# Kernel optimization log

Hardware: AMD Instinct MI355X
Metric: run time of the kernel (lower is better)

The kernel has to match this reference:

```python
import jax, jax.numpy as jnp
import numpy as np

N = 100000
E = 1600000
IN_CH = 165
H1 = 128
H2 = 64
OUT = 2


def gcn_conv(x, W, b, src, dst, n):
    # PyG GCNConv: linear transform, add self-loops, symmetric normalization,
    # scatter-add aggregation, then bias.
    h = x @ W  # [n, out_ch]
    ones = jnp.ones(src.shape[0], dtype=h.dtype)
    deg = jax.ops.segment_sum(ones, dst, num_segments=n) + 1.0  # +1 for self-loop
    dinv = jax.lax.rsqrt(deg)
    norm = dinv[src] * dinv[dst]  # [E]
    agg = jax.ops.segment_sum(h[src] * norm[:, None], dst, num_segments=n)
    agg = agg + (dinv * dinv)[:, None] * h  # self-loop contribution
    return agg + b


def setup_inputs() -> dict:
    key = jax.random.key(0)
    ks = jax.random.split(key, 8)
    x = jax.random.normal(ks[0], (N, IN_CH), dtype=jnp.float32)
    edge_index = jax.random.randint(ks[1], (2, E), 0, N, dtype=jnp.int32)
    W1 = jax.random.normal(ks[2], (IN_CH, H1), dtype=jnp.float32) * (1.0 / np.sqrt(IN_CH))
    b1 = jnp.zeros((H1,), dtype=jnp.float32)
    W2 = jax.random.normal(ks[3], (H1, H2), dtype=jnp.float32) * (1.0 / np.sqrt(H1))
    b2 = jnp.zeros((H2,), dtype=jnp.float32)
    Wo = jax.random.normal(ks[4], (H2, OUT), dtype=jnp.float32) * (1.0 / np.sqrt(H2))
    bo = jnp.zeros((OUT,), dtype=jnp.float32)
    return {"x": x, "edge_index": edge_index, "W1": W1, "b1": b1,
            "W2": W2, "b2": b2, "Wo": Wo, "bo": bo}


def reference(x, edge_index, W1, b1, W2, b2, Wo, bo):
    src, dst = edge_index[0], edge_index[1]
    n = x.shape[0]
    h = jax.nn.relu(gcn_conv(x, W1, b1, src, dst, n))
    h = jax.nn.relu(gcn_conv(h, W2, b2, src, dst, n))
    return h @ Wo + bo  # [N, 2] logits
```

## Files before the change

### kernel.cpp

```cpp
#include <hip/hip_runtime.h>
#include <hip/hip_fp16.h>

#define N_NODES 100000
#define N_EDGES 1600000
#define IN_CH 165
#define H1C 128
#define H2C 64
#define K1PAD 192
#define CAP 64
#define SCATTER_BLOCKS 2048
#define PART_SZ 12500
#define GEMM1_BLOCKS ((N_NODES + 63) / 64)

typedef _Float16 half8 __attribute__((ext_vector_type(8)));
typedef float floatx4 __attribute__((ext_vector_type(4)));

__global__ __launch_bounds__(256) void prep(const float* __restrict__ W1,
                                            const float* __restrict__ W2,
                                            int* __restrict__ cnt,
                                            _Float16* __restrict__ w1t,
                                            _Float16* __restrict__ w2t) {
    int i = blockIdx.x * 256 + threadIdx.x;
    if (i < N_NODES) cnt[i] = 0;
    if (i < H1C * K1PAD) {
        int c = i / K1PAD, k = i - c * K1PAD;
        w1t[i] = (k < IN_CH) ? (_Float16)W1[k * H1C + c] : (_Float16)0.0f;
    }
    if (i < H2C * H1C) {
        int c = i >> 7, k = i & 127;
        w2t[i] = (_Float16)W2[k * H2C + c];
    }
}

__global__ void dinv_from_cnt(const int* __restrict__ cnt, float* __restrict__ dinv) {
    int i = blockIdx.x * 256 + threadIdx.x;
    if (i < N_NODES) dinv[i] = rsqrtf((float)cnt[i] + 1.0f);
}

__global__ __launch_bounds__(256) void scatter_and_gemm1(
        const int* __restrict__ ei, int* __restrict__ cnt, int* __restrict__ csr,
        const float* __restrict__ x, const _Float16* __restrict__ w1t,
        _Float16* __restrict__ h1) {
    __shared__ _Float16 lsA[64 * 200];
    int tid = threadIdx.x;

    if (blockIdx.x < SCATTER_BLOCKS) {
        int g  = blockIdx.x & 7;
        int bg = blockIdx.x >> 3;
        int lo = g * PART_SZ;
        int hi = lo + PART_SZ;
        const int* dstp = ei + N_EDGES;
        for (int e = bg * 256 + tid; e < N_EDGES; e += (SCATTER_BLOCKS / 8) * 256) {
            int d = dstp[e];
            if (d >= lo && d < hi) {
                int s = ei[e];
                int pos = atomicAdd(&cnt[d], 1);
                if (pos < CAP) csr[(d << 6) + pos] = s;
            }
        }
        return;
    }

    int bid = blockIdx.x - SCATTER_BLOCKS;
    int row0 = bid * 64;

    const int TILE_EL = 64 * IN_CH;
    int base = row0 * IN_CH;
    for (int idx = tid; idx < TILE_EL; idx += 256) {
        int r = idx / IN_CH;
        int k = idx - r * IN_CH;
        int g = base + idx;
        float v = (g < N_NODES * IN_CH) ? x[g] : 0.0f;
        lsA[r * 200 + k] = (_Float16)v;
    }
    for (int idx = tid; idx < 64 * 35; idx += 256) {
        int r = idx / 35;
        int k = IN_CH + (idx - r * 35);
        lsA[r * 200 + k] = (_Float16)0.0f;
    }
    __syncthreads();

    int lane = tid & 63;
    int w = tid >> 6;
    int m = lane & 15;
    int q = lane >> 4;

    floatx4 acc[4][2] = {};
#pragma unroll
    for (int ks = 0; ks < 6; ++ks) {
        half8 af[4];
#pragma unroll
        for (int mt = 0; mt < 4; ++mt)
            af[mt] = *(const half8*)&lsA[(mt * 16 + m) * 200 + ks * 32 + q * 8];
        half8 bf[2];
#pragma unroll
        for (int nt = 0; nt < 2; ++nt)
            bf[nt] = *(const half8*)&w1t[((w * 2 + nt) * 16 + m) * K1PAD + ks * 32 + q * 8];
#pragma unroll
        for (int mt = 0; mt < 4; ++mt)
#pragma unroll
            for (int nt = 0; nt < 2; ++nt)
                acc[mt][nt] = __builtin_amdgcn_mfma_f32_16x16x32_f16(af[mt], bf[nt], acc[mt][nt], 0, 0, 0);
    }

#pragma unroll
    for (int mt = 0; mt < 4; ++mt) {
#pragma unroll
        for (int nt = 0; nt < 2; ++nt) {
            int col = (w * 2 + nt) * 16 + m;
#pragma unroll
            for (int reg = 0; reg < 4; ++reg) {
                int row = row0 + mt * 16 + q * 4 + reg;
                if (row < N_NODES) h1[(size_t)row * H1C + col] = (_Float16)acc[mt][nt][reg];
            }
        }
    }
}

__global__ __launch_bounds__(256) void gemm2_mfma(const _Float16* __restrict__ A,
                                                  const _Float16* __restrict__ w2t,
                                                  _Float16* __restrict__ h2) {
    __shared__ _Float16 lsA[64 * 136];
    int tid = threadIdx.x;
    int row0 = blockIdx.x * 64;

    const uint* srcu = (const uint*)(A + (size_t)row0 * H1C);
    for (int idx = tid; idx < 4096; idx += 256) {
        int r = idx >> 6;
        int kp = idx & 63;
        uint v = ((size_t)(row0 + r) < (size_t)N_NODES) ? srcu[idx] : 0u;
        *(uint*)&lsA[r * 136 + kp * 2] = v;
    }
    __syncthreads();

    int lane = tid & 63;
    int w = tid >> 6;
    int m = lane & 15;
    int q = lane >> 4;

    floatx4 acc[4] = {};
#pragma unroll
    for (int ks = 0; ks < 4; ++ks) {
        half8 bf = *(const half8*)&w2t[(w * 16 + m) * H1C + ks * 32 + q * 8];
#pragma unroll
        for (int mt = 0; mt < 4; ++mt) {
            half8 af = *(const half8*)&lsA[(mt * 16 + m) * 136 + ks * 32 + q * 8];
            acc[mt] = __builtin_amdgcn_mfma_f32_16x16x32_f16(af, bf, acc[mt], 0, 0, 0);
        }
    }

    int col = w * 16 + m;
#pragma unroll
    for (int mt = 0; mt < 4; ++mt) {
#pragma unroll
        for (int reg = 0; reg < 4; ++reg) {
            int row = row0 + mt * 16 + q * 4 + reg;
            if (row < N_NODES) h2[(size_t)row * H2C + col] = (_Float16)acc[mt][reg];
        }
    }
}

__global__ __launch_bounds__(256) void agg_gather_128(const __half* __restrict__ h,
                                                      const float* __restrict__ dinv,
                                                      const int* __restrict__ cnt,
                                                      const int* __restrict__ csr,
                                                      const float* __restrict__ b,
                                                      __half* __restrict__ out) {
    const __half2* hp = (const __half2*)h;
    int wave = threadIdx.x >> 6;
    int lane = threadIdx.x & 63;
    int node = blockIdx.x * 4 + wave;
    if (node >= N_NODES) return;
    int deg = min(cnt[node], CAP);
    const int* cp = csr + ((size_t)node << 6);
    float di = dinv[node];
    float ax = 0.0f, ay = 0.0f;
    int e = 0;
    for (; e + 3 < deg; e += 4) {
        int s0 = cp[e], s1 = cp[e + 1], s2 = cp[e + 2], s3 = cp[e + 3];
        float n0 = dinv[s0], n1 = dinv[s1], n2 = dinv[s2], n3 = dinv[s3];
        float2 v0 = __half22float2(hp[(size_t)s0 * 64 + lane]);
        float2 v1 = __half22float2(hp[(size_t)s1 * 64 + lane]);
        float2 v2 = __half22float2(hp[(size_t)s2 * 64 + lane]);
        float2 v3 = __half22float2(hp[(size_t)s3 * 64 + lane]);
        ax += v0.x * n0 + v1.x * n1 + v2.x * n2 + v3.x * n3;
        ay += v0.y * n0 + v1.y * n1 + v2.y * n2 + v3.y * n3;
    }
    for (; e < deg; ++e) {
        int s0 = cp[e];
        float n0 = dinv[s0];
        float2 v0 = __half22float2(hp[(size_t)s0 * 64 + lane]);
        ax += v0.x * n0;
        ay += v0.y * n0;
    }
    float2 hv = __half22float2(hp[(size_t)node * 64 + lane]);
    float2 bv = *(const float2*)&b[lane * 2];
    float ox = fmaxf(ax * di + di * di * hv.x + bv.x, 0.0f);
    float oy = fmaxf(ay * di + di * di * hv.y + bv.y, 0.0f);
    ((__half2*)out)[(size_t)node * 64 + lane] = __floats2half2_rn(ox, oy);
}

__global__ __launch_bounds__(256) void agg_gather_64_final(const __half* __restrict__ h,
                                                           const float* __restrict__ dinv,
                                                           const int* __restrict__ cnt,
                                                           const int* __restrict__ csr,
                                                           const float* __restrict__ b,
                                                           const float* __restrict__ Wo,
                                                           const float* __restrict__ bo,
                                                           float* __restrict__ out) {
    int wave = threadIdx.x >> 6;
    int lane = threadIdx.x & 63;
    int node = blockIdx.x * 4 + wave;
    if (node >= N_NODES) return;
    int deg = min(cnt[node], CAP);
    const int* cp = csr + ((size_t)node << 6);
    float di = dinv[node];
    float acc = 0.0f;
    int e = 0;
    for (; e + 3 < deg; e += 4) {
        int s0 = cp[e], s1 = cp[e + 1], s2 = cp[e + 2], s3 = cp[e + 3];
        float n0 = dinv[s0], n1 = dinv[s1], n2 = dinv[s2], n3 = dinv[s3];
        float v0 = __half2float(h[(size_t)s0 * H2C + lane]);
        float v1 = __half2float(h[(size_t)s1 * H2C + lane]);
        float v2 = __half2float(h[(size_t)s2 * H2C + lane]);
        float v3 = __half2float(h[(size_t)s3 * H2C + lane]);
        acc += v0 * n0 + v1 * n1 + v2 * n2 + v3 * n3;
    }
    for (; e < deg; ++e) {
        int s0 = cp[e];
        acc += __half2float(h[(size_t)s0 * H2C + lane]) * dinv[s0];
    }
    float hv = __half2float(h[(size_t)node * H2C + lane]);
    float v = fmaxf(acc * di + di * di * hv + b[lane], 0.0f);
    float a0 = v * Wo[lane * 2];
    float a1 = v * Wo[lane * 2 + 1];
#pragma unroll
    for (int off = 32; off > 0; off >>= 1) {
        a0 += __shfl_down(a0, off, 64);
        a1 += __shfl_down(a1, off, 64);
    }
    if (lane == 0) {
        *(float2*)&out[(size_t)node * 2] = make_float2(a0 + bo[0], a1 + bo[1]);
    }
}

static inline char* align256(char* p) {
    return (char*)(((uintptr_t)p + 255) & ~(uintptr_t)255);
}

extern "C" void kernel_launch(void* const* d_in, const int* in_sizes, int n_in,
                              void* d_out, int out_size, void* d_ws, size_t ws_size,
                              hipStream_t stream) {
    const float* x  = (const float*)d_in[0];
    const int*   ei = (const int*)d_in[1];
    const float* W1 = (const float*)d_in[2];
    const float* b1 = (const float*)d_in[3];
    const float* W2 = (const float*)d_in[4];
    const float* b2 = (const float*)d_in[5];
    const float* Wo = (const float*)d_in[6];
    const float* bo = (const float*)d_in[7];
    float* out = (float*)d_out;

    char* wp = (char*)d_ws;
    int* cnt      = (int*)wp;        wp = align256(wp + sizeof(int) * N_NODES);
    int* csr      = (int*)wp;        wp = align256(wp + sizeof(int) * (size_t)N_NODES * CAP);
    float* dinv   = (float*)wp;      wp = align256(wp + sizeof(float) * N_NODES);
    _Float16* w1t = (_Float16*)wp;   wp = align256(wp + sizeof(_Float16) * H1C * K1PAD);
    _Float16* w2t = (_Float16*)wp;   wp = align256(wp + sizeof(_Float16) * H2C * H1C);
    _Float16* h1h = (_Float16*)wp;   wp = align256(wp + sizeof(_Float16) * (size_t)N_NODES * H1C);
    _Float16* a1h = (_Float16*)wp;   wp = align256(wp + sizeof(_Float16) * (size_t)N_NODES * H1C);
    _Float16* h2h = (_Float16*)wp;   wp = align256(wp + sizeof(_Float16) * (size_t)N_NODES * H2C);

    const int nb_n   = (N_NODES + 255) / 256;
    const int nb_nd4 = (N_NODES + 3) / 4;

    prep<<<nb_n, 256, 0, stream>>>(W1, W2, cnt, w1t, w2t);

    scatter_and_gemm1<<<SCATTER_BLOCKS + GEMM1_BLOCKS, 256, 0, stream>>>(
        ei, cnt, csr, x, w1t, h1h);

    dinv_from_cnt<<<nb_n, 256, 0, stream>>>(cnt, dinv);

    agg_gather_128<<<nb_nd4, 256, 0, stream>>>((const __half*)h1h, dinv, cnt, csr, b1,
                                               (__half*)a1h);

    gemm2_mfma<<<(N_NODES + 63) / 64, 256, 0, stream>>>(a1h, w2t, h2h);

    agg_gather_64_final<<<nb_nd4, 256, 0, stream>>>((const __half*)h2h, dinv, cnt, csr,
                                                    b2, Wo, bo, out);
}
```

Before: 389.6 us.

## Fuse layer-1 aggregation into GEMM2 and add nontemporal loads/stores

```diff
diff --git a/kernel.cpp b/kernel.cpp
--- a/kernel.cpp
+++ b/kernel.cpp
@@ -51,9 +51,9 @@
         int hi = lo + PART_SZ;
         const int* dstp = ei + N_EDGES;
         for (int e = bg * 256 + tid; e < N_EDGES; e += (SCATTER_BLOCKS / 8) * 256) {
-            int d = dstp[e];
+            int d = __builtin_nontemporal_load(&dstp[e]);
             if (d >= lo && d < hi) {
-                int s = ei[e];
+                int s = __builtin_nontemporal_load(&ei[e]);
                 int pos = atomicAdd(&cnt[d], 1);
                 if (pos < CAP) csr[(d << 6) + pos] = s;
             }
@@ -70,7 +70,7 @@
         int r = idx / IN_CH;
         int k = idx - r * IN_CH;
         int g = base + idx;
-        float v = (g < N_NODES * IN_CH) ? x[g] : 0.0f;
+        float v = (g < N_NODES * IN_CH) ? __builtin_nontemporal_load(&x[g]) : 0.0f;
         lsA[r * 200 + k] = (_Float16)v;
     }
     for (int idx = tid; idx < 64 * 35; idx += 256) {
@@ -111,29 +111,62 @@
 #pragma unroll
             for (int reg = 0; reg < 4; ++reg) {
                 int row = row0 + mt * 16 + q * 4 + reg;
-                if (row < N_NODES) h1[(size_t)row * H1C + col] = (_Float16)acc[mt][nt][reg];
+                if (row < N_NODES)
+                    __builtin_nontemporal_store((_Float16)acc[mt][nt][reg],
+                                                &h1[(size_t)row * H1C + col]);
             }
         }
     }
 }
 
-__global__ __launch_bounds__(256) void gemm2_mfma(const _Float16* __restrict__ A,
+__global__ __launch_bounds__(256) void agg1_gemm2(const __half* __restrict__ h,
+                                                  const float* __restrict__ dinv,
+                                                  const int* __restrict__ cnt,
+                                                  const int* __restrict__ csr,
+                                                  const float* __restrict__ b,
                                                   const _Float16* __restrict__ w2t,
                                                   _Float16* __restrict__ h2) {
     __shared__ _Float16 lsA[64 * 136];
+    const __half2* hp = (const __half2*)h;
     int tid = threadIdx.x;
+    int wave = tid >> 6;
+    int lane = tid & 63;
     int row0 = blockIdx.x * 64;
 
-    const uint* srcu = (const uint*)(A + (size_t)row0 * H1C);
-    for (int idx = tid; idx < 4096; idx += 256) {
-        int r = idx >> 6;
-        int kp = idx & 63;
-        uint v = ((size_t)(row0 + r) < (size_t)N_NODES) ? srcu[idx] : 0u;
-        *(uint*)&lsA[r * 136 + kp * 2] = v;
+    for (int i = 0; i < 16; ++i) {
+        int r = wave * 16 + i;
+        int node = row0 + r;
+        if (node >= N_NODES) break;
+        int deg = min(cnt[node], CAP);
+        const int* cp = csr + ((size_t)node << 6);
+        float di = dinv[node];
+        float ax = 0.0f, ay = 0.0f;
+        int e = 0;
+        for (; e + 3 < deg; e += 4) {
+            int s0 = cp[e], s1 = cp[e + 1], s2 = cp[e + 2], s3 = cp[e + 3];
+            float n0 = dinv[s0], n1 = dinv[s1], n2 = dinv[s2], n3 = dinv[s3];
+            float2 v0 = __half22float2(hp[(size_t)s0 * 64 + lane]);
+            float2 v1 = __half22float2(hp[(size_t)s1 * 64 + lane]);
+            float2 v2 = __half22float2(hp[(size_t)s2 * 64 + lane]);
+            float2 v3 = __half22float2(hp[(size_t)s3 * 64 + lane]);
+            ax += v0.x * n0 + v1.x * n1 + v2.x * n2 + v3.x * n3;
+            ay += v0.y * n0 + v1.y * n1 + v2.y * n2 + v3.y * n3;
+        }
+        for (; e < deg; ++e) {
+            int s0 = cp[e];
+            float n0 = dinv[s0];
+            float2 v0 = __half22float2(hp[(size_t)s0 * 64 + lane]);
+            ax += v0.x * n0;
+            ay += v0.y * n0;
+        }
+        float2 hv = __half22float2(hp[(size_t)node * 64 + lane]);
+        float2 bv = *(const float2*)&b[lane * 2];
+        float ox = fmaxf(ax * di + di * di * hv.x + bv.x, 0.0f);
+        float oy = fmaxf(ay * di + di * di * hv.y + bv.y, 0.0f);
+        *(__half2*)&lsA[r * 136 + lane * 2] = __floats2half2_rn(ox, oy);
     }
     __syncthreads();
 
-    int lane = tid & 63;
     int w = tid >> 6;
     int m = lane & 15;
     int q = lane >> 4;
@@ -158,46 +191,6 @@
             if (row < N_NODES) h2[(size_t)row * H2C + col] = (_Float16)acc[mt][reg];
         }
     }
-}
-
-__global__ __launch_bounds__(256) void agg_gather_128(const __half* __restrict__ h,
-                                                      const float* __restrict__ dinv,
-                                                      const int* __restrict__ cnt,
-                                                      const int* __restrict__ csr,
-                                                      const float* __restrict__ b,
-                                                      __half* __restrict__ out) {
-    const __half2* hp = (const __half2*)h;
-    int wave = threadIdx.x >> 6;
-    int lane = threadIdx.x & 63;
-    int node = blockIdx.x * 4 + wave;
-    if (node >= N_NODES) return;
-    int deg = min(cnt[node], CAP);
-    const int* cp = csr + ((size_t)node << 6);
-    float di = dinv[node];
-    float ax = 0.0f, ay = 0.0f;
-    int e = 0;
-    for (; e + 3 < deg; e += 4) {
-        int s0 = cp[e], s1 = cp[e + 1], s2 = cp[e + 2], s3 = cp[e + 3];
-        float n0 = dinv[s0], n1 = dinv[s1], n2 = dinv[s2], n3 = dinv[s3];
-        float2 v0 = __half22float2(hp[(size_t)s0 * 64 + lane]);
-        float2 v1 = __half22float2(hp[(size_t)s1 * 64 + lane]);
-        float2 v2 = __half22float2(hp[(size_t)s2 * 64 + lane]);
-        float2 v3 = __half22float2(hp[(size_t)s3 * 64 + lane]);
-        ax += v0.x * n0 + v1.x * n1 + v2.x * n2 + v3.x * n3;
-        ay += v0.y * n0 + v1.y * n1 + v2.y * n2 + v3.y * n3;
-    }
-    for (; e < deg; ++e) {
-        int s0 = cp[e];
-        float n0 = dinv[s0];
-        float2 v0 = __half22float2(hp[(size_t)s0 * 64 + lane]);
-        ax += v0.x * n0;
-        ay += v0.y * n0;
-    }
-    float2 hv = __half22float2(hp[(size_t)node * 64 + lane]);
-    float2 bv = *(const float2*)&b[lane * 2];
-    float ox = fmaxf(ax * di + di * di * hv.x + bv.x, 0.0f);
-    float oy = fmaxf(ay * di + di * di * hv.y + bv.y, 0.0f);
-    ((__half2*)out)[(size_t)node * 64 + lane] = __floats2half2_rn(ox, oy);
 }
 
 __global__ __launch_bounds__(256) void agg_gather_64_final(const __half* __restrict__ h,
@@ -268,7 +261,6 @@
     _Float16* w1t = (_Float16*)wp;   wp = align256(wp + sizeof(_Float16) * H1C * K1PAD);
     _Float16* w2t = (_Float16*)wp;   wp = align256(wp + sizeof(_Float16) * H2C * H1C);
     _Float16* h1h = (_Float16*)wp;   wp = align256(wp + sizeof(_Float16) * (size_t)N_NODES * H1C);
-    _Float16* a1h = (_Float16*)wp;   wp = align256(wp + sizeof(_Float16) * (size_t)N_NODES * H1C);
     _Float16* h2h = (_Float16*)wp;   wp = align256(wp + sizeof(_Float16) * (size_t)N_NODES * H2C);
 
     const int nb_n   = (N_NODES + 255) / 256;
@@ -281,10 +273,8 @@
 
     dinv_from_cnt<<<nb_n, 256, 0, stream>>>(cnt, dinv);
 
-    agg_gather_128<<<nb_nd4, 256, 0, stream>>>((const __half*)h1h, dinv, cnt, csr, b1,
-                                               (__half*)a1h);
-
-    gemm2_mfma<<<(N_NODES + 63) / 64, 256, 0, stream>>>(a1h, w2t, h2h);
+    agg1_gemm2<<<GEMM1_BLOCKS, 256, 0, stream>>>((const __half*)h1h, dinv, cnt, csr, b1,
+                                                 w2t, h2h);
 
     agg_gather_64_final<<<nb_nd4, 256, 0, stream>>>((const __half*)h2h, dinv, cnt, csr,
                                                     b2, Wo, bo, out);
```

After: 404.1 us. 1.04x slower.
